# Optimization experiments

Hardware: AMD Instinct MI355X
Metric: run time of the kernel (lower is better)

## Reference

```python
import jax, jax.numpy as jnp
import numpy as np

ROUTING_ITERATIONS = 3


def squash(x):
    # squared norm over the capsule output dim
    sq = jnp.sum(x * x, axis=-1, keepdims=True)
    scale = sq / (1.0 + sq)
    return scale * x / jnp.sqrt(sq)


def setup_inputs() -> dict:
    key = jax.random.key(0)
    k1, k2 = jax.random.split(key)
    B, N, IN_C, K, OUT_C = 256, 1152, 8, 10, 16
    u = jax.random.normal(k1, (B, N, IN_C), dtype=jnp.float32)
    W = jax.random.normal(k2, (K, N, IN_C, OUT_C), dtype=jnp.float32)
    return {"u": u, "W": W}


def reference(u, W):
    # u: [B, N, in_c]; W: [K, N, in_c, out_c]
    # torch: u_hat = matmul(u[None,:,:,None,:], W[:,None]) -> [K, B, N, 1, out_c]
    u_hat = jnp.einsum('bni,knio->kbno', u, W)  # [K, B, N, out_c]
    b_ij = jnp.zeros_like(u_hat)
    v_j = None
    for it in range(ROUTING_ITERATIONS):
        c_ij = jax.nn.softmax(b_ij, axis=2)               # softmax over N, per out_c channel
        s_j = jnp.sum(c_ij * u_hat, axis=2, keepdims=True)  # [K, B, 1, out_c]
        v_j = squash(s_j)
        if it < ROUTING_ITERATIONS - 1:
            a_ij = jnp.sum(u_hat * v_j, axis=-1, keepdims=True)  # [K, B, N, 1]
            b_ij = b_ij + a_ij
    # match torch output shape [K, B, 1, 1, out_c]
    return v_j[:, :, :, None, :]
```

## Files before the change

kernel.cpp:

```cpp
#include <hip/hip_runtime.h>
#include <hip/hip_fp16.h>

#define Bsz 256
#define Nn  1152
#define Kk  10
#define NT  384
#define NW  6

#define W_ELEMS (Kk*Nn*128)
#define U_ELEMS (Bsz*Nn*8)

__device__ __forceinline__ unsigned pkh2(float x, float y) {
    __half2 h = __floats2half2_rn(x, y);
    return *reinterpret_cast<unsigned*>(&h);
}
__device__ __forceinline__ float2 uph2(unsigned v) {
    __half2 h;
    *reinterpret_cast<unsigned*>(&h) = v;
    return __half22float2(h);
}
__device__ __forceinline__ void up8(const uint4 q, float f[8]) {
    float2 a = uph2(q.x), b = uph2(q.y), c = uph2(q.z), d = uph2(q.w);
    f[0]=a.x; f[1]=a.y; f[2]=b.x; f[3]=b.y; f[4]=c.x; f[5]=c.y; f[6]=d.x; f[7]=d.y;
}

__global__ void cvt_kernel(const float* __restrict__ W, const float* __restrict__ u,
                           __half2* __restrict__ Wh, __half2* __restrict__ uh) {
    const int idx = blockIdx.x * blockDim.x + threadIdx.x;
    const int wg = W_ELEMS / 8;
    const float4* p;
    __half2* o;
    if (idx < wg) {
        p = (const float4*)W + (size_t)idx * 2;
        o = Wh + (size_t)idx * 4;
    } else {
        const int j = idx - wg;
        p = (const float4*)u + (size_t)j * 2;
        o = uh + (size_t)j * 4;
    }
    const float4 a = p[0], b = p[1];
    o[0] = __floats2half2_rn(a.x, a.y);
    o[1] = __floats2half2_rn(a.z, a.w);
    o[2] = __floats2half2_rn(b.x, b.y);
    o[3] = __floats2half2_rn(b.z, b.w);
}

template<bool HALF>
__global__ __launch_bounds__(NT, 6)
void digitcaps_kernel(const float* __restrict__ u32, const float* __restrict__ W32,
                      const __half* __restrict__ uh, const __half* __restrict__ Wh,
                      float* __restrict__ out)
{
    const int t    = threadIdx.x;
    const int lane = t & 63;
    const int wav  = t >> 6;
    const int b    = blockIdx.x;
    const int k    = blockIdx.y;

    __shared__ unsigned uhS[Nn * 8];
    __shared__ __half   cS[Nn];
    __shared__ float    redS[NW * 17];
    __shared__ __align__(16) float vS[16];
    __shared__ float    mS;

    {
        const int oh   = t & 1;
        const int nsub = t >> 1;
        float sacc[8];
        #pragma unroll
        for (int o = 0; o < 8; ++o) sacc[o] = 0.f;
        for (int r = 0; r < 6; ++r) {
            const int n = r * 192 + nsub;
            float ua[8];
            if (HALF) {
                up8(*(const uint4*)(uh + ((size_t)b * Nn + n) * 8), ua);
            } else {
                const float4* up = (const float4*)(u32 + ((size_t)b * Nn + n) * 8);
                const float4 x0 = up[0], x1 = up[1];
                ua[0]=x0.x; ua[1]=x0.y; ua[2]=x0.z; ua[3]=x0.w;
                ua[4]=x1.x; ua[5]=x1.y; ua[6]=x1.z; ua[7]=x1.w;
            }
            float a0[8];
            #pragma unroll
            for (int o = 0; o < 8; ++o) a0[o] = 0.f;
            #pragma unroll
            for (int i = 0; i < 8; ++i) {
                float wv[8];
                if (HALF) {
                    up8(*(const uint4*)(Wh + ((size_t)(k * Nn + n)) * 128 + i * 16 + oh * 8), wv);
                } else {
                    const float4* wp = (const float4*)(W32 + ((size_t)k * Nn + n) * 128 + i * 16 + oh * 8);
                    const float4 w0 = wp[0], w1 = wp[1];
                    wv[0]=w0.x; wv[1]=w0.y; wv[2]=w0.z; wv[3]=w0.w;
                    wv[4]=w1.x; wv[5]=w1.y; wv[6]=w1.z; wv[7]=w1.w;
                }
                const float x = ua[i];
                #pragma unroll
                for (int o = 0; o < 8; ++o) a0[o] += x * wv[o];
            }
            *(uint4*)&uhS[n * 8 + oh * 4] =
                make_uint4(pkh2(a0[0], a0[1]), pkh2(a0[2], a0[3]),
                           pkh2(a0[4], a0[5]), pkh2(a0[6], a0[7]));
            #pragma unroll
            for (int o = 0; o < 8; ++o) sacc[o] += a0[o];
        }
        #pragma unroll
        for (int off = 2; off <= 32; off <<= 1)
            #pragma unroll
            for (int o = 0; o < 8; ++o) sacc[o] += __shfl_xor(sacc[o], off);
        if (lane < 2) {
            #pragma unroll
            for (int o = 0; o < 8; ++o) redS[wav * 17 + lane * 8 + o] = sacc[o];
        }
    }
    __syncthreads();

    float lg[3] = {0.f, 0.f, 0.f};
    float v0[16];
    const int j_s = lane & 7;
    const int g_s = lane >> 3;

    for (int it = 0; it < 3; ++it) {
        if (it > 0) {
            const float4* vp = (const float4*)vS;
            #pragma unroll
            for (int q4 = 0; q4 < 4; ++q4) *(float4*)&v0[4*q4] = vp[q4];
            #pragma unroll
            for (int r = 0; r < 3; ++r) {
                const int n = t + r * NT;
                float fa[8], fb[8];
                up8(*(const uint4*)&uhS[n * 8], fa);
                up8(*(const uint4*)&uhS[n * 8 + 4], fb);
                float acc = 0.f;
                #pragma unroll
                for (int o = 0; o < 8; ++o) acc += fa[o] * v0[o] + fb[o] * v0[8 + o];
                lg[r] += acc;
            }
            float m = fmaxf(fmaxf(lg[0], lg[1]), lg[2]);
            #pragma unroll
            for (int off = 1; off <= 32; off <<= 1) m = fmaxf(m, __shfl_xor(m, off));
            if (lane == 0) redS[wav] = m;
            __syncthreads();
            if (t == 0) {
                float mm = redS[0];
                for (int w = 1; w < NW; ++w) mm = fmaxf(mm, redS[w]);
                mS = mm;
            }
            __syncthreads();
            m = mS;
            cS[t]          = __float2half(__expf(lg[0] - m));
            cS[t + NT]     = __float2half(__expf(lg[1] - m));
            cS[t + 2*NT]   = __float2half(__expf(lg[2] - m));
            __syncthreads();
            float spx = 0.f, spy = 0.f, dp = 0.f;
            #pragma unroll
            for (int cc = 0; cc < 24; ++cc) {
                const int n = cc * 48 + wav * 8 + g_s;
                const float c = __half2float(cS[n]);
                const float2 f = uph2(uhS[n * 8 + j_s]);
                spx += c * f.x; spy += c * f.y; dp += c;
            }
            #pragma unroll
            for (int off = 8; off <= 32; off <<= 1) {
                spx += __shfl_xor(spx, off);
                spy += __shfl_xor(spy, off);
                dp  += __shfl_xor(dp,  off);
            }
            if (lane < 8) {
                redS[wav * 17 + 2*j_s    ] = spx;
                redS[wav * 17 + 2*j_s + 1] = spy;
            }
            if (lane == 0) redS[wav * 17 + 16] = dp;
            __syncthreads();
        }

        if (t < 16) {
            float s = 0.f;
            #pragma unroll
            for (int w = 0; w < NW; ++w) s += redS[w * 17 + t];
            float d;
            if (it == 0) d = (float)Nn;
            else {
                d = 0.f;
                #pragma unroll
                for (int w = 0; w < NW; ++w) d += redS[w * 17 + 16];
            }
            s /= d;
            float s2 = s * s;
            #pragma unroll
            for (int off = 1; off <= 8; off <<= 1) s2 += __shfl_xor(s2, off);
            const float scale = (s2 / (1.f + s2)) * rsqrtf(fmaxf(s2, 1e-30f));
            const float v = s * scale;
            vS[t] = v;
            if (it == 2) out[((size_t)k * Bsz + b) * 16 + t] = v;
        }
        __syncthreads();
    }
}

extern "C" void kernel_launch(void* const* d_in, const int* in_sizes, int n_in,
                              void* d_out, int out_size, void* d_ws, size_t ws_size,
                              hipStream_t stream) {
    const float* u = (const float*)d_in[0];
    const float* W = (const float*)d_in[1];
    float* out = (float*)d_out;
    const size_t need = (size_t)(W_ELEMS + U_ELEMS) * sizeof(__half);
    if (ws_size >= need) {
        __half* Wh = (__half*)d_ws;
        __half* uhp = (__half*)((char*)d_ws + (size_t)W_ELEMS * sizeof(__half));
        cvt_kernel<<<dim3((W_ELEMS + U_ELEMS) / 8 / 256), dim3(256), 0, stream>>>(
            W, u, (__half2*)Wh, (__half2*)uhp);
        digitcaps_kernel<true><<<dim3(Bsz, Kk), dim3(NT), 0, stream>>>(
            nullptr, nullptr, uhp, Wh, out);
    } else {
        digitcaps_kernel<false><<<dim3(Bsz, Kk), dim3(NT), 0, stream>>>(
            u, W, nullptr, nullptr, out);
    }
}
```

Before: 141.5 us.

## Use packed fp16 dot2 instructions with interleaved W layout for u_hat and logits

The conversion kernel now writes W as fp16 pairs interleaved across input channels (i, i+1) for each output channel, so the main kernel can compute u_hat with v_dot2 fp16 instructions accumulating in fp32 instead of unpacking to float and doing scalar FMAs. The agreement dot product in the routing loop also uses fdot2 on packed u_hat against a half-packed v. This cuts conversion and FMA instruction count in the compute-heavy prologue. In exchange it rounds v to fp16 and changes the conversion kernel's access pattern, which is now strided with 32 scattered 4-byte stores per thread.

```diff
diff --git a/kernel.cpp b/kernel.cpp
--- a/kernel.cpp
+++ b/kernel.cpp
@@ -10,6 +10,8 @@
 #define W_ELEMS (Kk*Nn*128)
 #define U_ELEMS (Bsz*Nn*8)
 
+typedef _Float16 v2h __attribute__((ext_vector_type(2)));
+
 __device__ __forceinline__ unsigned pkh2(float x, float y) {
     __half2 h = __floats2half2_rn(x, y);
     return *reinterpret_cast<unsigned*>(&h);
@@ -19,36 +21,61 @@
     *reinterpret_cast<unsigned*>(&h) = v;
     return __half22float2(h);
 }
-__device__ __forceinline__ void up8(const uint4 q, float f[8]) {
-    float2 a = uph2(q.x), b = uph2(q.y), c = uph2(q.z), d = uph2(q.w);
-    f[0]=a.x; f[1]=a.y; f[2]=b.x; f[3]=b.y; f[4]=c.x; f[5]=c.y; f[6]=d.x; f[7]=d.y;
-}
+
+#if __has_builtin(__builtin_amdgcn_fdot2)
+__device__ __forceinline__ float fdot2u(unsigned a, unsigned b, float c) {
+    union { unsigned u; v2h h; } ua, ub;
+    ua.u = a; ub.u = b;
+    return __builtin_amdgcn_fdot2(ua.h, ub.h, c, false);
+}
+#else
+__device__ __forceinline__ float fdot2u(unsigned a, unsigned b, float c) {
+    const float2 fa = uph2(a), fb = uph2(b);
+    return c + fa.x * fb.x + fa.y * fb.y;
+}
+#endif
 
 __global__ void cvt_kernel(const float* __restrict__ W, const float* __restrict__ u,
-                           __half2* __restrict__ Wh, __half2* __restrict__ uh) {
-    const int idx = blockIdx.x * blockDim.x + threadIdx.x;
-    const int wg = W_ELEMS / 8;
-    const float4* p;
-    __half2* o;
-    if (idx < wg) {
-        p = (const float4*)W + (size_t)idx * 2;
-        o = Wh + (size_t)idx * 4;
+                           unsigned* __restrict__ Wp, __half2* __restrict__ uh) {
+    if (blockIdx.x < 90) {
+        const int idx = blockIdx.x * 256 + threadIdx.x;
+        const int k  = idx / 2304;
+        const int r  = idx - k * 2304;
+        const int n  = r >> 1;
+        const int oh = r & 1;
+        const float* src = W + ((size_t)(k * Nn + n)) * 128 + oh * 8;
+        unsigned* dst = Wp + (size_t)idx * 32;
+        #pragma unroll
+        for (int i2 = 0; i2 < 4; ++i2) {
+            const float4 e0 = *(const float4*)(src + (2*i2  )*16);
+            const float4 e1 = *(const float4*)(src + (2*i2  )*16 + 4);
+            const float4 f0 = *(const float4*)(src + (2*i2+1)*16);
+            const float4 f1 = *(const float4*)(src + (2*i2+1)*16 + 4);
+            dst[i2*8+0] = pkh2(e0.x, f0.x);
+            dst[i2*8+1] = pkh2(e0.y, f0.y);
+            dst[i2*8+2] = pkh2(e0.z, f0.z);
+            dst[i2*8+3] = pkh2(e0.w, f0.w);
+            dst[i2*8+4] = pkh2(e1.x, f1.x);
+            dst[i2*8+5] = pkh2(e1.y, f1.y);
+            dst[i2*8+6] = pkh2(e1.z, f1.z);
+            dst[i2*8+7] = pkh2(e1.w, f1.w);
+        }
     } else {
-        const int j = idx - wg;
-        p = (const float4*)u + (size_t)j * 2;
-        o = uh + (size_t)j * 4;
-    }
-    const float4 a = p[0], b = p[1];
-    o[0] = __floats2half2_rn(a.x, a.y);
-    o[1] = __floats2half2_rn(a.z, a.w);
-    o[2] = __floats2half2_rn(b.x, b.y);
-    o[3] = __floats2half2_rn(b.z, b.w);
+        const int idx = (blockIdx.x - 90) * 256 + threadIdx.x;
+        const float4* p = (const float4*)u + (size_t)idx * 2;
+        __half2* o = uh + (size_t)idx * 4;
+        const float4 a = p[0], b = p[1];
+        o[0] = __floats2half2_rn(a.x, a.y);
+        o[1] = __floats2half2_rn(a.z, a.w);
+        o[2] = __floats2half2_rn(b.x, b.y);
+        o[3] = __floats2half2_rn(b.z, b.w);
+    }
 }
 
 template<bool HALF>
 __global__ __launch_bounds__(NT, 6)
 void digitcaps_kernel(const float* __restrict__ u32, const float* __restrict__ W32,
-                      const __half* __restrict__ uh, const __half* __restrict__ Wh,
+                      const __half* __restrict__ uh, const unsigned* __restrict__ Wp,
                       float* __restrict__ out)
 {
     const int t    = threadIdx.x;
@@ -71,32 +98,35 @@
         for (int o = 0; o < 8; ++o) sacc[o] = 0.f;
         for (int r = 0; r < 6; ++r) {
             const int n = r * 192 + nsub;
-            float ua[8];
+            float a0[8];
+            #pragma unroll
+            for (int o = 0; o < 8; ++o) a0[o] = 0.f;
             if (HALF) {
-                up8(*(const uint4*)(uh + ((size_t)b * Nn + n) * 8), ua);
+                const uint4* wp8 = (const uint4*)Wp
+                                 + ((size_t)((k * Nn + n) * 2 + oh)) * 8;
+                uint4 wq[8];
+                #pragma unroll
+                for (int q = 0; q < 8; ++q) wq[q] = wp8[q];
+                const uint4 ubv = *(const uint4*)(uh + ((size_t)b * Nn + n) * 8);
+                const unsigned* u2v = (const unsigned*)&ubv;
+                const unsigned* wz  = (const unsigned*)wq;
+                #pragma unroll
+                for (int i2 = 0; i2 < 4; ++i2)
+                    #pragma unroll
+                    for (int o = 0; o < 8; ++o)
+                        a0[o] = fdot2u(u2v[i2], wz[i2*8 + o], a0[o]);
             } else {
                 const float4* up = (const float4*)(u32 + ((size_t)b * Nn + n) * 8);
                 const float4 x0 = up[0], x1 = up[1];
-                ua[0]=x0.x; ua[1]=x0.y; ua[2]=x0.z; ua[3]=x0.w;
-                ua[4]=x1.x; ua[5]=x1.y; ua[6]=x1.z; ua[7]=x1.w;
-            }
-            float a0[8];
-            #pragma unroll
-            for (int o = 0; o < 8; ++o) a0[o] = 0.f;
-            #pragma unroll
-            for (int i = 0; i < 8; ++i) {
-                float wv[8];
-                if (HALF) {
-                    up8(*(const uint4*)(Wh + ((size_t)(k * Nn + n)) * 128 + i * 16 + oh * 8), wv);
-                } else {
-                    const float4* wp = (const float4*)(W32 + ((size_t)k * Nn + n) * 128 + i * 16 + oh * 8);
-                    const float4 w0 = wp[0], w1 = wp[1];
-                    wv[0]=w0.x; wv[1]=w0.y; wv[2]=w0.z; wv[3]=w0.w;
-                    wv[4]=w1.x; wv[5]=w1.y; wv[6]=w1.z; wv[7]=w1.w;
+                float ua[8] = {x0.x,x0.y,x0.z,x0.w, x1.x,x1.y,x1.z,x1.w};
+                #pragma unroll
+                for (int i = 0; i < 8; ++i) {
+                    const float4* wpf = (const float4*)(W32 + ((size_t)k * Nn + n) * 128 + i * 16 + oh * 8);
+                    const float4 q0 = wpf[0], q1 = wpf[1];
+                    const float wvf[8] = {q0.x,q0.y,q0.z,q0.w, q1.x,q1.y,q1.z,q1.w};
+                    #pragma unroll
+                    for (int o = 0; o < 8; ++o) a0[o] += ua[i] * wvf[o];
                 }
-                const float x = ua[i];
-                #pragma unroll
-                for (int o = 0; o < 8; ++o) a0[o] += x * wv[o];
             }
             *(uint4*)&uhS[n * 8 + oh * 4] =
                 make_uint4(pkh2(a0[0], a0[1]), pkh2(a0[2], a0[3]),
@@ -116,24 +146,30 @@
     __syncthreads();
 
     float lg[3] = {0.f, 0.f, 0.f};
-    float v0[16];
+    unsigned vH[8];
     const int j_s = lane & 7;
     const int g_s = lane >> 3;
 
     for (int it = 0; it < 3; ++it) {
         if (it > 0) {
             const float4* vp = (const float4*)vS;
-            #pragma unroll
-            for (int q4 = 0; q4 < 4; ++q4) *(float4*)&v0[4*q4] = vp[q4];
+            const float4 va = vp[0], vb = vp[1], vc = vp[2], vd = vp[3];
+            vH[0] = pkh2(va.x, va.y); vH[1] = pkh2(va.z, va.w);
+            vH[2] = pkh2(vb.x, vb.y); vH[3] = pkh2(vb.z, vb.w);
+            vH[4] = pkh2(vc.x, vc.y); vH[5] = pkh2(vc.z, vc.w);
+            vH[6] = pkh2(vd.x, vd.y); vH[7] = pkh2(vd.z, vd.w);
             #pragma unroll
             for (int r = 0; r < 3; ++r) {
                 const int n = t + r * NT;
-                float fa[8], fb[8];
-                up8(*(const uint4*)&uhS[n * 8], fa);
-                up8(*(const uint4*)&uhS[n * 8 + 4], fb);
+                const uint4 qa = *(const uint4*)&uhS[n * 8];
+                const uint4 qb = *(const uint4*)&uhS[n * 8 + 4];
+                const unsigned* pa = (const unsigned*)&qa;
+                const unsigned* pb = (const unsigned*)&qb;
                 float acc = 0.f;
                 #pragma unroll
-                for (int o = 0; o < 8; ++o) acc += fa[o] * v0[o] + fb[o] * v0[8 + o];
+                for (int j = 0; j < 4; ++j) acc = fdot2u(pa[j], vH[j], acc);
+                #pragma unroll
+                for (int j = 0; j < 4; ++j) acc = fdot2u(pb[j], vH[4 + j], acc);
                 lg[r] += acc;
             }
             float m = fmaxf(fmaxf(lg[0], lg[1]), lg[2]);
@@ -148,9 +184,9 @@
             }
             __syncthreads();
             m = mS;
-            cS[t]          = __float2half(__expf(lg[0] - m));
-            cS[t + NT]     = __float2half(__expf(lg[1] - m));
-            cS[t + 2*NT]   = __float2half(__expf(lg[2] - m));
+            cS[t]        = __float2half(__expf(lg[0] - m));
+            cS[t + NT]   = __float2half(__expf(lg[1] - m));
+            cS[t + 2*NT] = __float2half(__expf(lg[2] - m));
             __syncthreads();
             float spx = 0.f, spy = 0.f, dp = 0.f;
             #pragma unroll
@@ -206,12 +242,12 @@
     float* out = (float*)d_out;
     const size_t need = (size_t)(W_ELEMS + U_ELEMS) * sizeof(__half);
     if (ws_size >= need) {
-        __half* Wh = (__half*)d_ws;
+        unsigned* Wp = (unsigned*)d_ws;
         __half* uhp = (__half*)((char*)d_ws + (size_t)W_ELEMS * sizeof(__half));
-        cvt_kernel<<<dim3((W_ELEMS + U_ELEMS) / 8 / 256), dim3(256), 0, stream>>>(
-            W, u, (__half2*)Wh, (__half2*)uhp);
+        cvt_kernel<<<dim3(90 + U_ELEMS / 8 / 256), dim3(256), 0, stream>>>(
+            W, u, Wp, (__half2*)uhp);
         digitcaps_kernel<true><<<dim3(Bsz, Kk), dim3(NT), 0, stream>>>(
-            nullptr, nullptr, uhp, Wh, out);
+            nullptr, nullptr, uhp, Wp, out);
     } else {
         digitcaps_kernel<false><<<dim3(Bsz, Kk), dim3(NT), 0, stream>>>(
             u, W, nullptr, nullptr, out);
```

Measured after the change: 178.7 us. 26.3% more time.
